# Optimization experiments

Hardware: AMD Instinct MI355X
Metric: run time of the kernel (lower is better)

## Reference

```python
import jax, jax.numpy as jnp
import numpy as np

IOU_THR = 0.5
SCORE_THR = 0.05
K = 1000  # fixed NMS candidate budget (padded-ragged replacement for data-dependent shapes)
BBOX_XFORM_CLIP = float(np.log(1000.0 / 16.0))  # torchvision BoxCoder clamp


def setup_inputs() -> dict:
    key = jax.random.key(0)
    k1, k2, k3, k4 = jax.random.split(key, 4)
    B, N, C = 8, 50000, 80
    pred_labels = jax.random.normal(k1, (B, N, C), jnp.float32)
    pred_bboxes = 0.5 * jax.random.normal(k2, (B, N, 4), jnp.float32)
    # anchors: valid xyxy boxes on a ~640px image
    cxy = jax.random.uniform(k3, (B, N, 2), jnp.float32, minval=0.0, maxval=640.0)
    wh = jax.random.uniform(k4, (B, N, 2), jnp.float32, minval=8.0, maxval=128.0)
    anchors = jnp.concatenate([cxy - 0.5 * wh, cxy + 0.5 * wh], axis=-1)
    return {"pred_labels": pred_labels, "pred_bboxes": pred_bboxes, "anchors": anchors}


def _decode_boxes(codes, anchors):
    # torchvision BoxCoder.decode_single with weights (1,1,1,1)
    w = anchors[:, 2] - anchors[:, 0]
    h = anchors[:, 3] - anchors[:, 1]
    cx = anchors[:, 0] + 0.5 * w
    cy = anchors[:, 1] + 0.5 * h
    dx, dy = codes[:, 0], codes[:, 1]
    dw = jnp.minimum(codes[:, 2], BBOX_XFORM_CLIP)
    dh = jnp.minimum(codes[:, 3], BBOX_XFORM_CLIP)
    pcx = dx * w + cx
    pcy = dy * h + cy
    pw = jnp.exp(dw) * w
    ph = jnp.exp(dh) * h
    return jnp.stack([pcx - 0.5 * pw, pcy - 0.5 * ph, pcx + 0.5 * pw, pcy + 0.5 * ph], axis=-1)


def _pairwise_iou(b):
    # b: [K,4] xyxy
    area = (b[:, 2] - b[:, 0]) * (b[:, 3] - b[:, 1])
    lt = jnp.maximum(b[:, None, :2], b[None, :, :2])
    rb = jnp.minimum(b[:, None, 2:], b[None, :, 2:])
    wh = jnp.clip(rb - lt, 0.0)
    inter = wh[..., 0] * wh[..., 1]
    return inter / (area[:, None] + area[None, :] - inter + 1e-9)


def _nms_keep(boxes):
    # boxes already sorted by descending score; greedy suppression
    iou = _pairwise_iou(boxes)
    idx = jnp.arange(K)

    def body(i, keep):
        suppress = (iou[i] > IOU_THR) & (idx > i) & keep[i]
        return keep & ~suppress

    return jax.lax.fori_loop(0, K, body, jnp.ones((K,), bool))


def _decode_image(labels, codes, anchors):
    # labels [N,C], codes [N,4], anchors [N,4]
    probs = jax.nn.sigmoid(labels)
    dt_score = jnp.max(probs, axis=1)
    dt_class = jnp.argmax(probs, axis=1)
    fg = (dt_class != 0) & (dt_score > SCORE_THR)
    masked = jnp.where(fg, dt_score, -1.0)  # background sorts last
    top_s, top_i = jax.lax.top_k(masked, K)
    cls = dt_class[top_i]
    boxes = _decode_boxes(codes[top_i], anchors[top_i])
    keep = _nms_keep(boxes) & (top_s > 0.0)
    out_scores = jnp.where(keep, top_s, 0.0)
    out_boxes = jnp.where(keep[:, None], boxes, 0.0)
    out_cls = jnp.where(keep, cls, -1)
    return out_cls, out_scores, out_boxes, keep


def reference(pred_labels, pred_bboxes, anchors):
    # Padded-ragged analog of the nested_tensor result:
    # category_ids [B,K] int, scores [B,K], bboxes [B,K,4], keep [B,K] validity mask
    return jax.vmap(_decode_image)(pred_labels, pred_bboxes, anchors)
```

## Files before the change

kernel.cpp:

```cpp
#include <hip/hip_runtime.h>
#include <cstdint>
#include <cstddef>

typedef unsigned int u32;
typedef unsigned long long u64;

#define BB   8
#define NN   50000
#define CC   80
#define KTOP 1000
#define CAP  4096
#define NHB  129
#define CLIPV 4.135166556742356f

#define OFF_KEYS 0UL
#define OFF_CLS  1600000UL
#define OFF_HIST 3200000UL
#define OFF_CNT  3204128UL
#define OFF_META 3204640UL
#define OFF_CAND 3204704UL
#define OFF_TKEY 3466848UL
#define OFF_TIDX 3498848UL
#define OFF_BOX  3530848UL
#define OFF_AREA 3658848UL
#define OFF_MAT  3690848UL
#define OFF_KEEP 4714848UL

__global__ __launch_bounds__(256) void k_scores_u(const float4* __restrict__ labels4,
                                                  u32* __restrict__ keys,
                                                  int* __restrict__ cls,
                                                  u32* __restrict__ ghist) {
    __shared__ float4 tile[64 * 21];
    __shared__ float  pbest[3][64];
    __shared__ int    pcls[3][64];
    __shared__ u32    lhist[NHB];
    int t = threadIdx.x;
    int img = blockIdx.x / 196;
    int blk = blockIdx.x - img * 196;
    size_t img_base = (size_t)img * NN * 20;
    for (int i = t; i < NHB; i += 256) lhist[i] = 0;
    int a = t & 63;
    int q = t >> 6;
#pragma unroll
    for (int tl = 0; tl < 4; ++tl) {
        int na0 = blk * 256 + tl * 64;
        int nv = NN - na0; if (nv > 64) nv = 64; if (nv < 0) nv = 0;
        int lim = nv * 20;
#pragma unroll
        for (int i = 0; i < 5; ++i) {
            int s = i * 256 + t;
            if (s < lim) {
                float4 v = labels4[img_base + (size_t)na0 * 20 + s];
                tile[s + s / 20] = v;
            }
        }
        __syncthreads();
        float best = -1.0e30f; int bc = 0;
        if (a < nv) {
#pragma unroll
            for (int j = 0; j < 5; ++j) {
                float4 v = tile[a * 21 + q * 5 + j];
                int c = q * 20 + j * 4;
                if (v.x > best) { best = v.x; bc = c; }
                if (v.y > best) { best = v.y; bc = c + 1; }
                if (v.z > best) { best = v.z; bc = c + 2; }
                if (v.w > best) { best = v.w; bc = c + 3; }
            }
            if (q > 0) { pbest[q - 1][a] = best; pcls[q - 1][a] = bc; }
        }
        __syncthreads();
        if (q == 0 && a < nv) {
#pragma unroll
            for (int r = 0; r < 3; ++r) {
                float pb = pbest[r][a];
                if (pb > best) { best = pb; bc = pcls[r][a]; }
            }
            int g = img * NN + na0 + a;
            float score = 1.0f / (1.0f + expf(-best));
            bool fg = (bc != 0) && (score > 0.05f);
            u32 key = fg ? __float_as_uint(score) : 0u;
            keys[g] = key;
            cls[g] = bc;
            u32 kb = key >> 16;
            u32 idx = (kb >= 0x3F00u) ? (kb - 0x3F00u) : 128u;
            atomicAdd(&lhist[idx], 1u);
        }
        __syncthreads();
    }
    for (int i = t; i < NHB; i += 256) {
        u32 c = lhist[i];
        if (c) atomicAdd(&ghist[img * NHB + i], c);
    }
}

__global__ __launch_bounds__(64) void k_thresh(const u32* __restrict__ ghist,
                                               u32* __restrict__ meta) {
    int b = blockIdx.x;
    if (threadIdx.x == 0) {
        const u32* h = ghist + b * NHB;
        u32 cum = 0; u32 t16 = 1u;
        for (int i = 127; i >= 0; --i) {
            cum += h[i];
            if (cum >= KTOP) { t16 = 0x3F00u + (u32)i; break; }
        }
        meta[b * 2] = t16; meta[b * 2 + 1] = 0;
    }
}

__global__ __launch_bounds__(256) void k_gather(const u32* __restrict__ keys,
                                                const u32* __restrict__ meta,
                                                u32* __restrict__ cnt,
                                                u64* __restrict__ cand) {
    __shared__ u32 wsum[4];
    __shared__ u32 bbase;
    int t = threadIdx.x;
    int img = blockIdx.x / 196;
    int blk = blockIdx.x - img * 196;
    int n = blk * 256 + t;
    u32 T16 = meta[img * 2];
    u32 key = 0; bool pass = false;
    if (n < NN) {
        key = keys[img * NN + n];
        pass = (key >> 16) >= T16;
    }
    u64 mask = __ballot(pass);
    int lane = t & 63, wid = t >> 6;
    u32 prefix = (u32)__popcll(mask & ((1ull << lane) - 1ull));
    if (lane == 0) wsum[wid] = (u32)__popcll(mask);
    __syncthreads();
    if (t == 0) {
        u32 s0 = wsum[0], s1 = wsum[1], s2 = wsum[2], s3 = wsum[3];
        u32 tot = s0 + s1 + s2 + s3;
        bbase = tot ? atomicAdd(&cnt[img * 16], tot) : 0u;
        wsum[0] = 0; wsum[1] = s0; wsum[2] = s0 + s1; wsum[3] = s0 + s1 + s2;
    }
    __syncthreads();
    if (pass) {
        u32 pos = bbase + wsum[wid] + prefix;
        if (pos < CAP)
            cand[(size_t)img * CAP + pos] = ((u64)key << 32) | (u32)(~(u32)n);
    }
}

__global__ __launch_bounds__(1024) void k_sort(const u64* __restrict__ cand,
                                               const u32* __restrict__ cnt,
                                               const float4* __restrict__ codes,
                                               const float4* __restrict__ anchors,
                                               u32* __restrict__ tkey, u32* __restrict__ tidx,
                                               float4* __restrict__ boxes, float* __restrict__ area) {
    __shared__ u64 sm[CAP];
    int b = blockIdx.x, tid = threadIdx.x;
    int m = (int)min(cnt[b * 16], (u32)CAP);
    for (int i = tid; i < CAP; i += 1024) sm[i] = (i < m) ? cand[(size_t)b * CAP + i] : 0ull;
    __syncthreads();
    for (int k = 2; k <= CAP; k <<= 1)
        for (int j = k >> 1; j > 0; j >>= 1) {
            for (int t = tid; t < CAP; t += 1024) {
                int ixj = t ^ j;
                if (ixj > t) {
                    u64 x = sm[t], y = sm[ixj];
                    bool desc = ((t & k) == 0);
                    if (desc ? (x < y) : (x > y)) { sm[t] = y; sm[ixj] = x; }
                }
            }
            __syncthreads();
        }
    if (tid < KTOP) {
        u64 v = sm[tid];
        u32 kb = (u32)(v >> 32);
        u32 n = ~(u32)v;
        if (kb == 0u) n = 0u;
        int g = b * KTOP + tid;
        tkey[g] = kb; tidx[g] = n;
        float4 a = anchors[(size_t)b * NN + n];
        float4 c = codes[(size_t)b * NN + n];
        float w = a.z - a.x, h = a.w - a.y;
        float cx = a.x + 0.5f * w, cy = a.y + 0.5f * h;
        float dw = fminf(c.z, CLIPV), dh = fminf(c.w, CLIPV);
        float pcx = c.x * w + cx, pcy = c.y * h + cy;
        float pw = expf(dw) * w, ph = expf(dh) * h;
        float x0 = pcx - 0.5f * pw, y0 = pcy - 0.5f * ph;
        float x1 = pcx + 0.5f * pw, y1 = pcy + 0.5f * ph;
        boxes[g] = make_float4(x0, y0, x1, y1);
        area[g] = (x1 - x0) * (y1 - y0);
    }
}

__global__ __launch_bounds__(256) void k_mat(const float4* __restrict__ boxes,
                                             const float* __restrict__ area,
                                             u64* __restrict__ mat) {
    __shared__ float4 sb[256];
    __shared__ float  sa[256];
    int bid = blockIdx.x;
    int wc = bid & 3, rc = (bid >> 2) & 3, b = bid >> 4;
    int t = threadIdx.x;
    int j0 = wc * 256;
    int jn = min(256, KTOP - j0);
    if (t < jn) { sb[t] = boxes[b * KTOP + j0 + t]; sa[t] = area[b * KTOP + j0 + t]; }
    __syncthreads();
    if (t >= 250) return;
    int i = rc * 250 + t;
    float4 bi = boxes[b * KTOP + i];
    float ai = area[b * KTOP + i];
    u64 w[4] = {0ull, 0ull, 0ull, 0ull};
    int estart = i - j0 + 1; if (estart < 0) estart = 0;
    for (int e = estart; e < jn; ++e) {
        float4 bj = sb[e];
        float lx = fmaxf(bi.x, bj.x), ly = fmaxf(bi.y, bj.y);
        float rx = fminf(bi.z, bj.z), ry = fminf(bi.w, bj.w);
        float ww = fmaxf(rx - lx, 0.0f), hh = fmaxf(ry - ly, 0.0f);
        float inter = ww * hh;
        float iou = inter / (ai + sa[e] - inter + 1e-9f);
        if (iou > 0.5f) w[e >> 6] |= (1ull << (e & 63));
    }
    u64* out = &mat[((size_t)(b * KTOP + i)) * 16 + wc * 4];
    out[0] = w[0]; out[1] = w[1]; out[2] = w[2]; out[3] = w[3];
}

__global__ __launch_bounds__(64) void k_nms(const u64* __restrict__ mat,
                                            u64* __restrict__ keepw) {
    __shared__ u64 buf[2][1024];
    int b = blockIdx.x, lane = threadIdx.x;
    const u64* mb = mat + (size_t)b * (KTOP * 16);
#pragma unroll
    for (int r = 0; r < 16; ++r) buf[0][r * 64 + lane] = mb[r * 64 + lane];
    __syncthreads();
    u64 kw = 0;
    if (lane < 15) kw = ~0ull;
    else if (lane == 15) kw = (1ull << 40) - 1;
    for (int p = 0; p < 16; ++p) {
        int cur = p & 1;
        u64 stg[16];
        if (p < 15) {
#pragma unroll
            for (int r = 0; r < 16; ++r) {
                int idx = (p + 1) * 1024 + r * 64 + lane;
                stg[r] = (idx < KTOP * 16) ? mb[idx] : 0ull;
            }
        }
        u64 applied = 0;
        if (lane == p) {
            for (int c = 0; c < 8; ++c) {
                u64 col[8];
#pragma unroll
                for (int qq = 0; qq < 8; ++qq) col[qq] = buf[cur][(c * 8 + qq) * 16 + p];
#pragma unroll
                for (int qq = 0; qq < 8; ++qq) {
                    int e = c * 8 + qq;
                    if ((kw >> e) & 1ull) { kw &= ~col[qq]; applied |= (1ull << e); }
                }
            }
        }
        applied = __shfl(applied, p);
        if (lane > p && lane < 16) {
            for (int c = 0; c < 8; ++c) {
                u64 col[8];
#pragma unroll
                for (int qq = 0; qq < 8; ++qq) col[qq] = buf[cur][(c * 8 + qq) * 16 + lane];
#pragma unroll
                for (int qq = 0; qq < 8; ++qq)
                    if ((applied >> (c * 8 + qq)) & 1ull) kw &= ~col[qq];
            }
        }
        __syncthreads();
        if (p < 15) {
#pragma unroll
            for (int r = 0; r < 16; ++r) buf[cur ^ 1][r * 64 + lane] = stg[r];
            __syncthreads();
        }
    }
    if (lane < 16) keepw[b * 16 + lane] = kw;
}

__global__ __launch_bounds__(256) void k_out(const u64* __restrict__ keepw,
                                             const u32* __restrict__ tkey,
                                             const u32* __restrict__ tidx,
                                             const int* __restrict__ cls,
                                             const float4* __restrict__ boxes,
                                             float* __restrict__ out) {
    int gid = blockIdx.x * 256 + threadIdx.x;
    if (gid >= BB * KTOP) return;
    int b = gid / KTOP;
    int k = gid - b * KTOP;
    u64 kwv = keepw[b * 16 + (k >> 6)];
    bool kp = (kwv >> (k & 63)) & 1ull;
    float sc = __uint_as_float(tkey[gid]);
    kp = kp && (sc > 0.0f);
    int cl = cls[(size_t)b * NN + tidx[gid]];
    float4 bx = boxes[gid];
    const int BK = BB * KTOP;
    out[gid] = kp ? (float)cl : -1.0f;
    out[BK + gid] = kp ? sc : 0.0f;
    float* ob = out + 2 * BK + (size_t)gid * 4;
    ob[0] = kp ? bx.x : 0.0f;
    ob[1] = kp ? bx.y : 0.0f;
    ob[2] = kp ? bx.z : 0.0f;
    ob[3] = kp ? bx.w : 0.0f;
    out[6 * BK + gid] = kp ? 1.0f : 0.0f;
}

extern "C" void kernel_launch(void* const* d_in, const int* in_sizes, int n_in,
                              void* d_out, int out_size, void* d_ws, size_t ws_size,
                              hipStream_t stream) {
    const float* labels  = (const float*)d_in[0];
    const float* codes   = (const float*)d_in[1];
    const float* anchors = (const float*)d_in[2];
    char* ws = (char*)d_ws;
    u32* keys  = (u32*)(ws + OFF_KEYS);
    int* cls   = (int*)(ws + OFF_CLS);
    u32* hist  = (u32*)(ws + OFF_HIST);
    u32* cnt   = (u32*)(ws + OFF_CNT);
    u32* meta  = (u32*)(ws + OFF_META);
    u64* cand  = (u64*)(ws + OFF_CAND);
    u32* tkey  = (u32*)(ws + OFF_TKEY);
    u32* tidx  = (u32*)(ws + OFF_TIDX);
    float4* bx = (float4*)(ws + OFF_BOX);
    float* ar  = (float*)(ws + OFF_AREA);
    u64* mat   = (u64*)(ws + OFF_MAT);
    u64* kpw   = (u64*)(ws + OFF_KEEP);

    hipMemsetAsync(ws + OFF_HIST, 0, OFF_CAND - OFF_HIST, stream);

    k_scores_u<<<BB * 196, 256, 0, stream>>>((const float4*)labels, keys, cls, hist);
    k_thresh<<<BB, 64, 0, stream>>>(hist, meta);
    k_gather<<<BB * 196, 256, 0, stream>>>(keys, meta, cnt, cand);
    k_sort<<<BB, 1024, 0, stream>>>(cand, cnt, (const float4*)codes, (const float4*)anchors,
                                    tkey, tidx, bx, ar);
    k_mat<<<BB * 16, 256, 0, stream>>>(bx, ar, mat);
    k_nms<<<BB, 64, 0, stream>>>(mat, kpw);
    k_out<<<(BB * KTOP + 255) / 256, 256, 0, stream>>>(kpw, tkey, tidx, cls, bx, (float*)d_out);
}
```

Measured before the change: 375.9 us.

## Fuse threshold into gather, split bitonic sort across blocks, fuse NMS with output

The single-thread threshold kernel is removed. Each gather block now recomputes the histogram threshold with a wave-level prefix scan. The 4096-element bitonic sort is split in two: 32 blocks sort 1024-element chunks in alternating directions, then one 512-thread block per image runs the final two merge stages, so the early stages spread across more CUs. The output writing is folded into the NMS kernel to drop a launch and the keep-word round trip through global memory, at the cost of serial output work in 64-thread blocks.

```diff
diff --git a/kernel.cpp b/kernel.cpp
--- a/kernel.cpp
+++ b/kernel.cpp
@@ -17,14 +17,12 @@
 #define OFF_CLS  1600000UL
 #define OFF_HIST 3200000UL
 #define OFF_CNT  3204128UL
-#define OFF_META 3204640UL
-#define OFF_CAND 3204704UL
-#define OFF_TKEY 3466848UL
-#define OFF_TIDX 3498848UL
-#define OFF_BOX  3530848UL
-#define OFF_AREA 3658848UL
-#define OFF_MAT  3690848UL
-#define OFF_KEEP 4714848UL
+#define OFF_CAND 3204640UL
+#define OFF_TKEY 3466784UL
+#define OFF_TIDX 3498784UL
+#define OFF_BOX  3530784UL
+#define OFF_AREA 3658784UL
+#define OFF_MAT  3690784UL
 
 __global__ __launch_bounds__(256) void k_scores_u(const float4* __restrict__ labels4,
                                                   u32* __restrict__ keys,
@@ -93,31 +91,38 @@
     }
 }
 
-__global__ __launch_bounds__(64) void k_thresh(const u32* __restrict__ ghist,
-                                               u32* __restrict__ meta) {
-    int b = blockIdx.x;
-    if (threadIdx.x == 0) {
-        const u32* h = ghist + b * NHB;
-        u32 cum = 0; u32 t16 = 1u;
-        for (int i = 127; i >= 0; --i) {
-            cum += h[i];
-            if (cum >= KTOP) { t16 = 0x3F00u + (u32)i; break; }
-        }
-        meta[b * 2] = t16; meta[b * 2 + 1] = 0;
-    }
-}
-
 __global__ __launch_bounds__(256) void k_gather(const u32* __restrict__ keys,
-                                                const u32* __restrict__ meta,
+                                                const u32* __restrict__ ghist,
                                                 u32* __restrict__ cnt,
                                                 u64* __restrict__ cand) {
     __shared__ u32 wsum[4];
     __shared__ u32 bbase;
+    __shared__ u32 sT16;
+    __shared__ u32 wtot;
     int t = threadIdx.x;
     int img = blockIdx.x / 196;
     int blk = blockIdx.x - img * 196;
+
+    u32 v = 0;
+    if (t < 128) v = ghist[img * NHB + (127 - t)];
+    u32 incl = v;
+#pragma unroll
+    for (int d = 1; d < 64; d <<= 1) {
+        u32 up = __shfl_up(incl, (unsigned)d);
+        if ((t & 63) >= d) incl += up;
+    }
+    if (t == 63) wtot = incl;
+    __syncthreads();
+    if (t >= 64 && t < 128) incl += wtot;
+    if (t < 128) {
+        u32 excl = incl - v;
+        if (excl < KTOP && incl >= KTOP) sT16 = 0x3F00u + 127u - (u32)t;
+    }
+    if (t == 127 && incl < KTOP) sT16 = 0x3F00u;
+    __syncthreads();
+    u32 T16 = sT16;
+
     int n = blk * 256 + t;
-    u32 T16 = meta[img * 2];
     u32 key = 0; bool pass = false;
     if (n < NN) {
         key = keys[img * NN + n];
@@ -142,47 +147,79 @@
     }
 }
 
-__global__ __launch_bounds__(1024) void k_sort(const u64* __restrict__ cand,
-                                               const u32* __restrict__ cnt,
+__global__ __launch_bounds__(256) void k_sortA(u64* __restrict__ cand,
+                                               const u32* __restrict__ cnt) {
+    __shared__ u64 sm[1024];
+    int b = blockIdx.x >> 2;
+    int c = blockIdx.x & 3;
+    int tid = threadIdx.x;
+    int m = (int)min(cnt[b * 16], (u32)CAP);
+    int base = c * 1024;
+    u64* cp = cand + (size_t)b * CAP;
+    for (int i = tid; i < 1024; i += 256) {
+        int g = base + i;
+        sm[i] = (g < m) ? cp[g] : 0ull;
+    }
+    __syncthreads();
+    for (int k = 2; k <= 1024; k <<= 1)
+        for (int j = k >> 1; j > 0; j >>= 1) {
+            for (int i = tid; i < 1024; i += 256) {
+                int ixj = i ^ j;
+                if (ixj > i) {
+                    bool desc = (((base + i) & k) == 0);
+                    u64 x = sm[i], y = sm[ixj];
+                    if (desc ? (x < y) : (x > y)) { sm[i] = y; sm[ixj] = x; }
+                }
+            }
+            __syncthreads();
+        }
+    for (int i = tid; i < 1024; i += 256) cp[base + i] = sm[i];
+}
+
+__global__ __launch_bounds__(512) void k_sortB(const u64* __restrict__ cand,
                                                const float4* __restrict__ codes,
                                                const float4* __restrict__ anchors,
                                                u32* __restrict__ tkey, u32* __restrict__ tidx,
                                                float4* __restrict__ boxes, float* __restrict__ area) {
     __shared__ u64 sm[CAP];
     int b = blockIdx.x, tid = threadIdx.x;
-    int m = (int)min(cnt[b * 16], (u32)CAP);
-    for (int i = tid; i < CAP; i += 1024) sm[i] = (i < m) ? cand[(size_t)b * CAP + i] : 0ull;
-    __syncthreads();
-    for (int k = 2; k <= CAP; k <<= 1)
+    const u64* cp = cand + (size_t)b * CAP;
+    for (int i = tid; i < CAP; i += 512) sm[i] = cp[i];
+    __syncthreads();
+    for (int k = 2048; k <= 4096; k <<= 1)
         for (int j = k >> 1; j > 0; j >>= 1) {
-            for (int t = tid; t < CAP; t += 1024) {
-                int ixj = t ^ j;
-                if (ixj > t) {
-                    u64 x = sm[t], y = sm[ixj];
-                    bool desc = ((t & k) == 0);
-                    if (desc ? (x < y) : (x > y)) { sm[t] = y; sm[ixj] = x; }
+            for (int i = tid; i < CAP; i += 512) {
+                int ixj = i ^ j;
+                if (ixj > i) {
+                    bool desc = ((i & k) == 0);
+                    u64 x = sm[i], y = sm[ixj];
+                    if (desc ? (x < y) : (x > y)) { sm[i] = y; sm[ixj] = x; }
                 }
             }
             __syncthreads();
         }
-    if (tid < KTOP) {
-        u64 v = sm[tid];
-        u32 kb = (u32)(v >> 32);
-        u32 n = ~(u32)v;
-        if (kb == 0u) n = 0u;
-        int g = b * KTOP + tid;
-        tkey[g] = kb; tidx[g] = n;
-        float4 a = anchors[(size_t)b * NN + n];
-        float4 c = codes[(size_t)b * NN + n];
-        float w = a.z - a.x, h = a.w - a.y;
-        float cx = a.x + 0.5f * w, cy = a.y + 0.5f * h;
-        float dw = fminf(c.z, CLIPV), dh = fminf(c.w, CLIPV);
-        float pcx = c.x * w + cx, pcy = c.y * h + cy;
-        float pw = expf(dw) * w, ph = expf(dh) * h;
-        float x0 = pcx - 0.5f * pw, y0 = pcy - 0.5f * ph;
-        float x1 = pcx + 0.5f * pw, y1 = pcy + 0.5f * ph;
-        boxes[g] = make_float4(x0, y0, x1, y1);
-        area[g] = (x1 - x0) * (y1 - y0);
+#pragma unroll
+    for (int r = 0; r < 2; ++r) {
+        int i = r * 512 + tid;
+        if (i < KTOP) {
+            u64 v = sm[i];
+            u32 kb = (u32)(v >> 32);
+            u32 n = ~(u32)v;
+            if (kb == 0u) n = 0u;
+            int g = b * KTOP + i;
+            tkey[g] = kb; tidx[g] = n;
+            float4 a = anchors[(size_t)b * NN + n];
+            float4 cc = codes[(size_t)b * NN + n];
+            float w = a.z - a.x, h = a.w - a.y;
+            float cx = a.x + 0.5f * w, cy = a.y + 0.5f * h;
+            float dw = fminf(cc.z, CLIPV), dh = fminf(cc.w, CLIPV);
+            float pcx = cc.x * w + cx, pcy = cc.y * h + cy;
+            float pw = expf(dw) * w, ph = expf(dh) * h;
+            float x0 = pcx - 0.5f * pw, y0 = pcy - 0.5f * ph;
+            float x1 = pcx + 0.5f * pw, y1 = pcy + 0.5f * ph;
+            boxes[g] = make_float4(x0, y0, x1, y1);
+            area[g] = (x1 - x0) * (y1 - y0);
+        }
     }
 }
 
@@ -213,13 +250,18 @@
         float iou = inter / (ai + sa[e] - inter + 1e-9f);
         if (iou > 0.5f) w[e >> 6] |= (1ull << (e & 63));
     }
-    u64* out = &mat[((size_t)(b * KTOP + i)) * 16 + wc * 4];
-    out[0] = w[0]; out[1] = w[1]; out[2] = w[2]; out[3] = w[3];
-}
-
-__global__ __launch_bounds__(64) void k_nms(const u64* __restrict__ mat,
-                                            u64* __restrict__ keepw) {
+    u64* outp = &mat[((size_t)(b * KTOP + i)) * 16 + wc * 4];
+    outp[0] = w[0]; outp[1] = w[1]; outp[2] = w[2]; outp[3] = w[3];
+}
+
+__global__ __launch_bounds__(64) void k_nmsout(const u64* __restrict__ mat,
+                                               const u32* __restrict__ tkey,
+                                               const u32* __restrict__ tidx,
+                                               const int* __restrict__ cls,
+                                               const float4* __restrict__ boxes,
+                                               float* __restrict__ out) {
     __shared__ u64 buf[2][1024];
+    __shared__ u64 kws[16];
     int b = blockIdx.x, lane = threadIdx.x;
     const u64* mb = mat + (size_t)b * (KTOP * 16);
 #pragma unroll
@@ -269,34 +311,29 @@
             __syncthreads();
         }
     }
-    if (lane < 16) keepw[b * 16 + lane] = kw;
-}
-
-__global__ __launch_bounds__(256) void k_out(const u64* __restrict__ keepw,
-                                             const u32* __restrict__ tkey,
-                                             const u32* __restrict__ tidx,
-                                             const int* __restrict__ cls,
-                                             const float4* __restrict__ boxes,
-                                             float* __restrict__ out) {
-    int gid = blockIdx.x * 256 + threadIdx.x;
-    if (gid >= BB * KTOP) return;
-    int b = gid / KTOP;
-    int k = gid - b * KTOP;
-    u64 kwv = keepw[b * 16 + (k >> 6)];
-    bool kp = (kwv >> (k & 63)) & 1ull;
-    float sc = __uint_as_float(tkey[gid]);
-    kp = kp && (sc > 0.0f);
-    int cl = cls[(size_t)b * NN + tidx[gid]];
-    float4 bx = boxes[gid];
+    if (lane < 16) kws[lane] = kw;
+    __syncthreads();
     const int BK = BB * KTOP;
-    out[gid] = kp ? (float)cl : -1.0f;
-    out[BK + gid] = kp ? sc : 0.0f;
-    float* ob = out + 2 * BK + (size_t)gid * 4;
-    ob[0] = kp ? bx.x : 0.0f;
-    ob[1] = kp ? bx.y : 0.0f;
-    ob[2] = kp ? bx.z : 0.0f;
-    ob[3] = kp ? bx.w : 0.0f;
-    out[6 * BK + gid] = kp ? 1.0f : 0.0f;
+#pragma unroll
+    for (int r = 0; r < 16; ++r) {
+        int k = r * 64 + lane;
+        if (k < KTOP) {
+            int g = b * KTOP + k;
+            bool kp = (kws[k >> 6] >> (k & 63)) & 1ull;
+            float sc = __uint_as_float(tkey[g]);
+            kp = kp && (sc > 0.0f);
+            int cl = cls[(size_t)b * NN + tidx[g]];
+            float4 bx = boxes[g];
+            out[g] = kp ? (float)cl : -1.0f;
+            out[BK + g] = kp ? sc : 0.0f;
+            float* ob = out + 2 * BK + (size_t)g * 4;
+            ob[0] = kp ? bx.x : 0.0f;
+            ob[1] = kp ? bx.y : 0.0f;
+            ob[2] = kp ? bx.z : 0.0f;
+            ob[3] = kp ? bx.w : 0.0f;
+            out[6 * BK + g] = kp ? 1.0f : 0.0f;
+        }
+    }
 }
 
 extern "C" void kernel_launch(void* const* d_in, const int* in_sizes, int n_in,
@@ -310,23 +347,20 @@
     int* cls   = (int*)(ws + OFF_CLS);
     u32* hist  = (u32*)(ws + OFF_HIST);
     u32* cnt   = (u32*)(ws + OFF_CNT);
-    u32* meta  = (u32*)(ws + OFF_META);
     u64* cand  = (u64*)(ws + OFF_CAND);
     u32* tkey  = (u32*)(ws + OFF_TKEY);
     u32* tidx  = (u32*)(ws + OFF_TIDX);
     float4* bx = (float4*)(ws + OFF_BOX);
     float* ar  = (float*)(ws + OFF_AREA);
     u64* mat   = (u64*)(ws + OFF_MAT);
-    u64* kpw   = (u64*)(ws + OFF_KEEP);
 
     hipMemsetAsync(ws + OFF_HIST, 0, OFF_CAND - OFF_HIST, stream);
 
     k_scores_u<<<BB * 196, 256, 0, stream>>>((const float4*)labels, keys, cls, hist);
-    k_thresh<<<BB, 64, 0, stream>>>(hist, meta);
-    k_gather<<<BB * 196, 256, 0, stream>>>(keys, meta, cnt, cand);
-    k_sort<<<BB, 1024, 0, stream>>>(cand, cnt, (const float4*)codes, (const float4*)anchors,
+    k_gather<<<BB * 196, 256, 0, stream>>>(keys, hist, cnt, cand);
+    k_sortA<<<BB * 4, 256, 0, stream>>>(cand, cnt);
+    k_sortB<<<BB, 512, 0, stream>>>(cand, (const float4*)codes, (const float4*)anchors,
                                     tkey, tidx, bx, ar);
     k_mat<<<BB * 16, 256, 0, stream>>>(bx, ar, mat);
-    k_nms<<<BB, 64, 0, stream>>>(mat, kpw);
-    k_out<<<(BB * KTOP + 255) / 256, 256, 0, stream>>>(kpw, tkey, tidx, cls, bx, (float*)d_out);
-}
+    k_nmsout<<<BB, 64, 0, stream>>>(mat, tkey, tidx, cls, bx, (float*)d_out);
+}
```

Result: slower. 388.7 us (+3.4%).
